# Kernel tuning notes

Measured on AMD Instinct MI355X. Metric: run time of the kernel, lower is better.

The kernel has to match this reference:

```python
import jax, jax.numpy as jnp
import numpy as np

C = 8.0


def _linear_scan(alpha, xbeta):
    # h_t = alpha_t * h_{t-1} + xbeta_t, scan over time axis=1
    def combine(e1, e2):
        a1, b1 = e1
        a2, b2 = e2
        return a2 * a1, a2 * b1 + b2
    _, h = jax.lax.associative_scan(combine, (alpha, xbeta), axis=1)
    return h


def setup_inputs() -> dict:
    dim = 2048
    B, T = 4, 4096
    key = jax.random.key(0)
    k_x, k_wi, k_wg = jax.random.split(key, 3)
    std = dim ** -0.5
    x = jax.random.normal(k_x, (B, T, dim), dtype=jnp.float32)
    W_in = jax.random.normal(k_wi, (dim, dim), dtype=jnp.float32) * std
    b_in = jnp.zeros((dim,), dtype=jnp.float32)
    W_gate = jax.random.normal(k_wg, (dim, dim), dtype=jnp.float32) * std
    b_gate = jnp.zeros((dim,), dtype=jnp.float32)
    forget_lambda = jnp.linspace(-4.323, -9.0, dim, dtype=jnp.float32)
    return {"x": x, "W_in": W_in, "b_in": b_in, "W_gate": W_gate,
            "b_gate": b_gate, "forget_lambda": forget_lambda}


def reference(x, W_in, b_in, W_gate, b_gate, forget_lambda):
    # x: [B, T, D]
    input_gate = jnp.einsum('btd,ed->bte', x, W_in) + b_in
    recurrence_gate = jnp.einsum('btd,ed->bte', x, W_gate) + b_gate
    # alpha_t = exp(-C * softplus(lambda) * sigmoid(r_t))  per channel
    alpha = jnp.exp(-C * jax.nn.softplus(forget_lambda) * jax.nn.sigmoid(recurrence_gate))
    beta = jnp.sqrt(1.0 - alpha ** 2 + 1e-6)
    xbeta = beta * jax.nn.sigmoid(input_gate) * x
    return _linear_scan(alpha, xbeta)
```

## Files before the change

kernel.cpp:

```cpp
#include <hip/hip_runtime.h>

typedef unsigned short u16;
typedef unsigned int u32;

using bf16x8 = __attribute__((ext_vector_type(8))) __bf16;
using f32x4  = __attribute__((ext_vector_type(4))) float;
using u16x8  = __attribute__((ext_vector_type(8))) u16;

#define BB 4
#define TT 4096
#define DD 2048
#define MM 16384
#define KK 2048
#define NCHUNK 16
#define CLEN 256

__device__ __forceinline__ u16 f2bf(float f) {
    u32 u = __float_as_uint(f);
    u32 r = (u + 0x7FFFu + ((u >> 16) & 1u)) >> 16;
    return (u16)r;
}

__device__ __forceinline__ void gload_lds16(const void* g, void* l) {
    __builtin_amdgcn_global_load_lds(
        (const __attribute__((address_space(1))) void*)g,
        (__attribute__((address_space(3))) void*)l, 16, 0, 0);
}

__global__ __launch_bounds__(256) void cvt_kernel(const float* __restrict__ in,
                                                  u16* __restrict__ out, int n8) {
    int i = blockIdx.x * 256 + threadIdx.x;
    if (i >= n8) return;
    const f32x4* p = (const f32x4*)in + (size_t)i * 2;
    f32x4 a = p[0], b = p[1];
    u16x8 o;
    o[0] = f2bf(a[0]); o[1] = f2bf(a[1]); o[2] = f2bf(a[2]); o[3] = f2bf(a[3]);
    o[4] = f2bf(b[0]); o[5] = f2bf(b[1]); o[6] = f2bf(b[2]); o[7] = f2bf(b[3]);
    *((u16x8*)out + i) = o;
}

#define BM 128
#define BN 128
#define BKg 32

__global__ __launch_bounds__(512) void gemm_dual(
    const u16* __restrict__ xb, const u16* __restrict__ wib, const u16* __restrict__ wgb,
    const float* __restrict__ xf,
    const float* __restrict__ b_in, const float* __restrict__ b_gate,
    const float* __restrict__ lam, u32* __restrict__ pair)
{
    __shared__ u16 As[BM * BKg];
    __shared__ u16 Bi[BN * BKg];
    __shared__ u16 Bg[BN * BKg];

    int tid = threadIdx.x;
    int bid = blockIdx.x;
    int cpx = gridDim.x >> 3;
    int swz = (bid & 7) * cpx + (bid >> 3);
    int et = swz & 15;
    int mt = swz >> 4;

    size_t m0 = (size_t)mt * BM;
    size_t e0 = (size_t)et * BN;

    int lane = tid & 63;
    int wid = tid >> 6;
    int wr  = wid >> 2;
    int wc  = wid & 3;

    int srow = tid >> 2;
    int skp  = (tid & 3) << 3;
    const u16* ga = xb  + (m0 + srow) * KK + skp;
    const u16* gi = wib + (e0 + srow) * KK + skp;
    const u16* gg = wgb + (e0 + srow) * KK + skp;
    u16* la = &As[tid * 8];
    u16* li = &Bi[tid * 8];
    u16* lg = &Bg[tid * 8];

    f32x4 accI[4][2], accG[4][2];
#pragma unroll
    for (int i = 0; i < 4; i++)
#pragma unroll
        for (int j = 0; j < 2; j++) {
            accI[i][j] = (f32x4){0.f, 0.f, 0.f, 0.f};
            accG[i][j] = (f32x4){0.f, 0.f, 0.f, 0.f};
        }

    int rowIn16 = lane & 15;
    int ksel = (lane >> 4) << 3;

    for (int k0 = 0; k0 < KK; k0 += BKg) {
        gload_lds16(ga, la);
        gload_lds16(gi, li);
        gload_lds16(gg, lg);
        ga += BKg; gi += BKg; gg += BKg;
        __syncthreads();

        bf16x8 aF[4], iF[2], gF[2];
#pragma unroll
        for (int mi = 0; mi < 4; mi++)
            aF[mi] = *(const bf16x8*)&As[(wr * 64 + mi * 16 + rowIn16) * BKg + ksel];
#pragma unroll
        for (int ni = 0; ni < 2; ni++) {
            iF[ni] = *(const bf16x8*)&Bi[(wc * 32 + ni * 16 + rowIn16) * BKg + ksel];
            gF[ni] = *(const bf16x8*)&Bg[(wc * 32 + ni * 16 + rowIn16) * BKg + ksel];
        }
#pragma unroll
        for (int mi = 0; mi < 4; mi++)
#pragma unroll
            for (int ni = 0; ni < 2; ni++) {
                accI[mi][ni] = __builtin_amdgcn_mfma_f32_16x16x32_bf16(aF[mi], iF[ni], accI[mi][ni], 0, 0, 0);
                accG[mi][ni] = __builtin_amdgcn_mfma_f32_16x16x32_bf16(aF[mi], gF[ni], accG[mi][ni], 0, 0, 0);
            }
        __syncthreads();
    }

    float spl[2], biv[2], bgv[2];
    size_t ecol[2];
#pragma unroll
    for (int ni = 0; ni < 2; ni++) {
        size_t e = e0 + wc * 32 + ni * 16 + rowIn16;
        ecol[ni] = e;
        spl[ni] = 8.0f * log1pf(__expf(lam[e]));
        biv[ni] = b_in[e];
        bgv[ni] = b_gate[e];
    }
    int rbase = (lane >> 4) * 4;
#pragma unroll
    for (int mi = 0; mi < 4; mi++) {
#pragma unroll
        for (int r = 0; r < 4; r++) {
            size_t m = m0 + wr * 64 + mi * 16 + rbase + r;
#pragma unroll
            for (int ni = 0; ni < 2; ni++) {
                size_t e = ecol[ni];
                float ig = accI[mi][ni][r] + biv[ni];
                float rg = accG[mi][ni][r] + bgv[ni];
                float sigr = 1.f / (1.f + __expf(-rg));
                float g = spl[ni] * sigr;
                float beta = sqrtf(1.f - __expf(-2.f * g) + 1e-6f);
                float xv = xf[m * DD + e];
                float xbeta = beta * (1.f / (1.f + __expf(-ig))) * xv;
                u32 pk = (u32)f2bf(g) | (((u32)f2bf(xbeta)) << 16);
                pair[m * DD + e] = pk;
            }
        }
    }
}

__global__ __launch_bounds__(256) void scanA(const u32* __restrict__ pair,
                                             float* __restrict__ aggG,
                                             float* __restrict__ aggB) {
    int gid = blockIdx.x * 256 + threadIdx.x;
    int e = gid & (DD - 1);
    int rest = gid >> 11;
    int b = rest & 3;
    int c = rest >> 2;
    const u32* p = pair + ((size_t)(b * TT + c * CLEN)) * DD + e;
    float gsum = 0.f, h = 0.f;
#pragma unroll 4
    for (int t = 0; t < CLEN; ++t) {
        u32 v = *p; p += DD;
        float gf = __uint_as_float(v << 16);
        float xbv = __uint_as_float(v & 0xFFFF0000u);
        gsum += gf;
        h = fmaf(__expf(-gf), h, xbv);
    }
    int idx = ((b * NCHUNK + c) << 11) | e;
    aggG[idx] = gsum;
    aggB[idx] = h;
}

__global__ __launch_bounds__(256) void scanB(const float* __restrict__ aggG,
                                             const float* __restrict__ aggB,
                                             float* __restrict__ carry) {
    int gid = blockIdx.x * 256 + threadIdx.x;
    int e = gid & (DD - 1);
    int b = gid >> 11;
    float h = 0.f;
#pragma unroll
    for (int c = 0; c < NCHUNK; ++c) {
        int idx = ((b * NCHUNK + c) << 11) | e;
        carry[idx] = h;
        h = fmaf(__expf(-aggG[idx]), h, aggB[idx]);
    }
}

__global__ __launch_bounds__(256) void scanC(const u32* __restrict__ pair,
                                             const float* __restrict__ carry,
                                             float* __restrict__ out) {
    int gid = blockIdx.x * 256 + threadIdx.x;
    int e = gid & (DD - 1);
    int rest = gid >> 11;
    int b = rest & 3;
    int c = rest >> 2;
    const u32* p = pair + ((size_t)(b * TT + c * CLEN)) * DD + e;
    float* o = out + ((size_t)(b * TT + c * CLEN)) * DD + e;
    float h = carry[((b * NCHUNK + c) << 11) | e];
#pragma unroll 4
    for (int t = 0; t < CLEN; ++t) {
        u32 v = *p; p += DD;
        float gf = __uint_as_float(v << 16);
        float xbv = __uint_as_float(v & 0xFFFF0000u);
        h = fmaf(__expf(-gf), h, xbv);
        *o = h; o += DD;
    }
}

extern "C" void kernel_launch(void* const* d_in, const int* in_sizes, int n_in,
                              void* d_out, int out_size, void* d_ws, size_t ws_size,
                              hipStream_t stream) {
    const float* x      = (const float*)d_in[0];
    const float* W_in   = (const float*)d_in[1];
    const float* b_in   = (const float*)d_in[2];
    const float* W_gate = (const float*)d_in[3];
    const float* b_gate = (const float*)d_in[4];
    const float* lam    = (const float*)d_in[5];
    float* out = (float*)d_out;

    char* ws = (char*)d_ws;
    u16* xb   = (u16*)(ws);
    u16* wib  = (u16*)(ws + 67108864);
    u16* wgb  = (u16*)(ws + 75497472);
    u32* pair = (u32*)(ws + 83886080);
    float* aggG  = (float*)(ws + 218103808);
    float* aggB  = (float*)(ws + 218628096);
    float* carry = (float*)(ws + 219152384);

    cvt_kernel<<<16384, 256, 0, stream>>>(x, xb, MM * KK / 8);
    cvt_kernel<<<2048, 256, 0, stream>>>(W_in, wib, DD * KK / 8);
    cvt_kernel<<<2048, 256, 0, stream>>>(W_gate, wgb, DD * KK / 8);
    gemm_dual<<<(MM / BM) * (DD / BN), 512, 0, stream>>>(xb, wib, wgb, x, b_in, b_gate, lam, pair);
    scanA<<<BB * DD * NCHUNK / 256, 256, 0, stream>>>(pair, aggG, aggB);
    scanB<<<BB * DD / 256, 256, 0, stream>>>(aggG, aggB, carry);
    scanC<<<BB * DD * NCHUNK / 256, 256, 0, stream>>>(pair, carry, out);
}
```

Before: 491.7 us.

## Rewrite dual GEMM with 4-stage LDS pipeline, larger M tile, swizzle

Replaces the single-buffered dual GEMM with a 256x128 tile that keeps a 4-deep ring of LDS buffers. Loads run three k-steps ahead, waits use explicit vmcnt/lgkmcnt counts, and each k-step's MFMA work is split into two halves that interleave with the async loads. The LDS layout is XOR-swizzled to avoid bank conflicts, and s_setprio is raised around the MFMA blocks. The aim is to hide global-load latency and raise the MFMA share of the loop. The cost is more LDS and registers per block (launch bounds ask for 2 blocks per CU) and fragile hand-placed wait counts.

```diff
diff --git a/kernel.cpp b/kernel.cpp
--- a/kernel.cpp
+++ b/kernel.cpp
@@ -26,6 +26,12 @@
         (const __attribute__((address_space(1))) void*)g,
         (__attribute__((address_space(3))) void*)l, 16, 0, 0);
 }
+
+#define BAR() do { __builtin_amdgcn_sched_barrier(0); __builtin_amdgcn_s_barrier(); __builtin_amdgcn_sched_barrier(0); } while(0)
+#define WAIT_LGKM0() do { asm volatile("s_waitcnt lgkmcnt(0)" ::: "memory"); __builtin_amdgcn_sched_barrier(0); } while(0)
+#define WAIT_VM8() do { asm volatile("s_waitcnt vmcnt(8)" ::: "memory"); __builtin_amdgcn_sched_barrier(0); } while(0)
+#define WAIT_VM4() do { asm volatile("s_waitcnt vmcnt(4)" ::: "memory"); __builtin_amdgcn_sched_barrier(0); } while(0)
+#define WAIT_VM0() do { asm volatile("s_waitcnt vmcnt(0)" ::: "memory"); __builtin_amdgcn_sched_barrier(0); } while(0)
 
 __global__ __launch_bounds__(256) void cvt_kernel(const float* __restrict__ in,
                                                   u16* __restrict__ out, int n8) {
@@ -39,98 +45,130 @@
     *((u16x8*)out + i) = o;
 }
 
-#define BM 128
-#define BN 128
+#define BMg 256
+#define BNg 128
 #define BKg 32
-
-__global__ __launch_bounds__(512) void gemm_dual(
+#define NT (KK / BKg)
+
+__global__ __launch_bounds__(512, 2) void gemm_dual8(
     const u16* __restrict__ xb, const u16* __restrict__ wib, const u16* __restrict__ wgb,
     const float* __restrict__ xf,
     const float* __restrict__ b_in, const float* __restrict__ b_gate,
     const float* __restrict__ lam, u32* __restrict__ pair)
 {
-    __shared__ u16 As[BM * BKg];
-    __shared__ u16 Bi[BN * BKg];
-    __shared__ u16 Bg[BN * BKg];
-
-    int tid = threadIdx.x;
-    int bid = blockIdx.x;
-    int cpx = gridDim.x >> 3;
-    int swz = (bid & 7) * cpx + (bid >> 3);
-    int et = swz & 15;
-    int mt = swz >> 4;
-
-    size_t m0 = (size_t)mt * BM;
-    size_t e0 = (size_t)et * BN;
-
-    int lane = tid & 63;
-    int wid = tid >> 6;
-    int wr  = wid >> 2;
-    int wc  = wid & 3;
-
-    int srow = tid >> 2;
-    int skp  = (tid & 3) << 3;
-    const u16* ga = xb  + (m0 + srow) * KK + skp;
-    const u16* gi = wib + (e0 + srow) * KK + skp;
-    const u16* gg = wgb + (e0 + srow) * KK + skp;
-    u16* la = &As[tid * 8];
-    u16* li = &Bi[tid * 8];
-    u16* lg = &Bg[tid * 8];
-
-    f32x4 accI[4][2], accG[4][2];
-#pragma unroll
-    for (int i = 0; i < 4; i++)
+    __shared__ u16 As[4][BMg * BKg];
+    __shared__ u16 Bs[4][2][BNg * BKg];
+
+    const int tid = threadIdx.x;
+    const int bid = blockIdx.x;
+    const int cpx = gridDim.x >> 3;
+    const int swz = (bid & 7) * cpx + (bid >> 3);
+    const int et = swz & 15;
+    const int mt = swz >> 4;
+    const size_t m0 = (size_t)mt * BMg;
+    const size_t e0 = (size_t)et * BNg;
+
+    const int lane = tid & 63;
+    const int wid = tid >> 6;
+    const int wr = wid >> 2;
+    const int wc = wid & 3;
+    const int r15 = lane & 15;
+    const int s4 = lane >> 4;
+
+    const int srow = tid >> 2;
+    const int sseg = (tid & 3) ^ ((tid >> 3) & 3);
+    const int skp  = sseg << 3;
+
+    const int koff = ((s4 ^ ((r15 >> 1) & 3)) << 3);
+
+#define STAGE_A(t) do { int _b = (t) & 3; size_t _k = (size_t)(t) * BKg + skp; \
+        gload_lds16(xb + (m0 + srow) * KK + _k,        &As[_b][tid * 8]); \
+        gload_lds16(xb + (m0 + 128 + srow) * KK + _k,  &As[_b][4096 + tid * 8]); } while (0)
+#define STAGE_B(t) do { int _b = (t) & 3; size_t _k = (size_t)(t) * BKg + skp; \
+        gload_lds16(wib + (e0 + srow) * KK + _k, &Bs[_b][0][tid * 8]); \
+        gload_lds16(wgb + (e0 + srow) * KK + _k, &Bs[_b][1][tid * 8]); } while (0)
+
+    f32x4 accI[8][2], accG[8][2];
+#pragma unroll
+    for (int i = 0; i < 8; i++)
 #pragma unroll
         for (int j = 0; j < 2; j++) {
             accI[i][j] = (f32x4){0.f, 0.f, 0.f, 0.f};
             accG[i][j] = (f32x4){0.f, 0.f, 0.f, 0.f};
         }
 
-    int rowIn16 = lane & 15;
-    int ksel = (lane >> 4) << 3;
-
-    for (int k0 = 0; k0 < KK; k0 += BKg) {
-        gload_lds16(ga, la);
-        gload_lds16(gi, li);
-        gload_lds16(gg, lg);
-        ga += BKg; gi += BKg; gg += BKg;
-        __syncthreads();
-
-        bf16x8 aF[4], iF[2], gF[2];
-#pragma unroll
-        for (int mi = 0; mi < 4; mi++)
-            aF[mi] = *(const bf16x8*)&As[(wr * 64 + mi * 16 + rowIn16) * BKg + ksel];
+    STAGE_A(0); STAGE_B(0);
+    STAGE_A(1); STAGE_B(1);
+    STAGE_A(2); STAGE_B(2);
+    WAIT_VM8();
+    BAR();
+
+    for (int t = 0; t < NT; ++t) {
+        const int cb = t & 3;
+        const u16* Ab = &As[cb][0];
+        const u16* BiB = &Bs[cb][0][0];
+        const u16* BgB = &Bs[cb][1][0];
+        bf16x8 bI[2], bG[2], aF[4];
+
+#pragma unroll
+        for (int q = 0; q < 4; q++)
+            aF[q] = *(const bf16x8*)&Ab[(wr * 128 + q * 16 + r15) * BKg + koff];
 #pragma unroll
         for (int ni = 0; ni < 2; ni++) {
-            iF[ni] = *(const bf16x8*)&Bi[(wc * 32 + ni * 16 + rowIn16) * BKg + ksel];
-            gF[ni] = *(const bf16x8*)&Bg[(wc * 32 + ni * 16 + rowIn16) * BKg + ksel];
+            bI[ni] = *(const bf16x8*)&BiB[(wc * 32 + ni * 16 + r15) * BKg + koff];
+            bG[ni] = *(const bf16x8*)&BgB[(wc * 32 + ni * 16 + r15) * BKg + koff];
         }
-#pragma unroll
-        for (int mi = 0; mi < 4; mi++)
+        if (t < NT - 3) STAGE_A(t + 3);
+        BAR();
+        WAIT_LGKM0();
+        __builtin_amdgcn_s_setprio(1);
+#pragma unroll
+        for (int q = 0; q < 4; q++)
 #pragma unroll
             for (int ni = 0; ni < 2; ni++) {
-                accI[mi][ni] = __builtin_amdgcn_mfma_f32_16x16x32_bf16(aF[mi], iF[ni], accI[mi][ni], 0, 0, 0);
-                accG[mi][ni] = __builtin_amdgcn_mfma_f32_16x16x32_bf16(aF[mi], gF[ni], accG[mi][ni], 0, 0, 0);
+                accI[q][ni] = __builtin_amdgcn_mfma_f32_16x16x32_bf16(aF[q], bI[ni], accI[q][ni], 0, 0, 0);
+                accG[q][ni] = __builtin_amdgcn_mfma_f32_16x16x32_bf16(aF[q], bG[ni], accG[q][ni], 0, 0, 0);
             }
-        __syncthreads();
+        __builtin_amdgcn_s_setprio(0);
+        BAR();
+
+#pragma unroll
+        for (int q = 0; q < 4; q++)
+            aF[q] = *(const bf16x8*)&Ab[(wr * 128 + (q + 4) * 16 + r15) * BKg + koff];
+        if (t < NT - 3) STAGE_B(t + 3);
+        BAR();
+        WAIT_LGKM0();
+        __builtin_amdgcn_s_setprio(1);
+#pragma unroll
+        for (int q = 0; q < 4; q++)
+#pragma unroll
+            for (int ni = 0; ni < 2; ni++) {
+                accI[q + 4][ni] = __builtin_amdgcn_mfma_f32_16x16x32_bf16(aF[q], bI[ni], accI[q + 4][ni], 0, 0, 0);
+                accG[q + 4][ni] = __builtin_amdgcn_mfma_f32_16x16x32_bf16(aF[q], bG[ni], accG[q + 4][ni], 0, 0, 0);
+            }
+        __builtin_amdgcn_s_setprio(0);
+        if (t < NT - 3)      WAIT_VM8();
+        else if (t == NT - 3) WAIT_VM4();
+        else                  WAIT_VM0();
+        BAR();
     }
 
     float spl[2], biv[2], bgv[2];
     size_t ecol[2];
 #pragma unroll
     for (int ni = 0; ni < 2; ni++) {
-        size_t e = e0 + wc * 32 + ni * 16 + rowIn16;
+        size_t e = e0 + wc * 32 + ni * 16 + r15;
         ecol[ni] = e;
         spl[ni] = 8.0f * log1pf(__expf(lam[e]));
         biv[ni] = b_in[e];
         bgv[ni] = b_gate[e];
     }
-    int rbase = (lane >> 4) * 4;
-#pragma unroll
-    for (int mi = 0; mi < 4; mi++) {
+    const int rbase = s4 * 4;
+#pragma unroll
+    for (int mi = 0; mi < 8; mi++) {
 #pragma unroll
         for (int r = 0; r < 4; r++) {
-            size_t m = m0 + wr * 64 + mi * 16 + rbase + r;
+            size_t m = m0 + wr * 128 + mi * 16 + rbase + r;
 #pragma unroll
             for (int ni = 0; ni < 2; ni++) {
                 size_t e = ecol[ni];
@@ -146,6 +184,8 @@
             }
         }
     }
+#undef STAGE_A
+#undef STAGE_B
 }
 
 __global__ __launch_bounds__(256) void scanA(const u32* __restrict__ pair,
@@ -230,7 +270,7 @@
     cvt_kernel<<<16384, 256, 0, stream>>>(x, xb, MM * KK / 8);
     cvt_kernel<<<2048, 256, 0, stream>>>(W_in, wib, DD * KK / 8);
     cvt_kernel<<<2048, 256, 0, stream>>>(W_gate, wgb, DD * KK / 8);
-    gemm_dual<<<(MM / BM) * (DD / BN), 512, 0, stream>>>(xb, wib, wgb, x, b_in, b_gate, lam, pair);
+    gemm_dual8<<<(MM / BMg) * (DD / BNg), 512, 0, stream>>>(xb, wib, wgb, x, b_in, b_gate, lam, pair);
     scanA<<<BB * DD * NCHUNK / 256, 256, 0, stream>>>(pair, aggG, aggB);
     scanB<<<BB * DD / 256, 256, 0, stream>>>(aggG, aggB, carry);
     scanC<<<BB * DD * NCHUNK / 256, 256, 0, stream>>>(pair, carry, out);
```

New measurement: 503.5 us. 2.4% more time.

## Interleave gate weights into one concatenated GEMM with 256x256 double-buffered tiles

Applied to the files above, without the earlier changes.

The two weight matrices are converted into a single interleaved bf16 matrix, so the dual GEMM becomes one GEMM of width 4096. It uses 256x256 tiles with a K step of 64, double-buffered LDS stages with an XOR swizzle, and a scheduled MFMA/LDS-read interleave. The epilogue pairs input-gate and recurrence-gate columns through a lane shuffle and reads x from the bf16 copy instead of the fp32 input. This aims at more data reuse per LDS load and fewer barriers. In exchange it needs large LDS (128KB) and many registers, which can limit occupancy, and x is now rounded to bf16 in the xbeta term.

```diff
diff --git a/kernel.cpp b/kernel.cpp
--- a/kernel.cpp
+++ b/kernel.cpp
@@ -12,6 +12,7 @@
 #define DD 2048
 #define MM 16384
 #define KK 2048
+#define NN 4096
 #define NCHUNK 16
 #define CLEN 256
 
@@ -39,113 +40,152 @@
     *((u16x8*)out + i) = o;
 }
 
-#define BM 128
-#define BN 128
-#define BKg 32
-
-__global__ __launch_bounds__(512) void gemm_dual(
-    const u16* __restrict__ xb, const u16* __restrict__ wib, const u16* __restrict__ wgb,
-    const float* __restrict__ xf,
+__global__ __launch_bounds__(256) void cvtw_kernel(const float* __restrict__ in,
+                                                   u16* __restrict__ out, int gate) {
+    int i = blockIdx.x * 256 + threadIdx.x;
+    int row = i >> 8;
+    int col8 = i & 255;
+    const f32x4* p = (const f32x4*)in + (size_t)i * 2;
+    f32x4 a = p[0], b = p[1];
+    u16x8 o;
+    o[0] = f2bf(a[0]); o[1] = f2bf(a[1]); o[2] = f2bf(a[2]); o[3] = f2bf(a[3]);
+    o[4] = f2bf(b[0]); o[5] = f2bf(b[1]); o[6] = f2bf(b[2]); o[7] = f2bf(b[3]);
+    size_t oidx = (((size_t)row * 2 + gate) << 11) + (size_t)col8 * 8;
+    *(u16x8*)(out + oidx) = o;
+}
+
+#define BKc 64
+#define NT (KK / BKc)
+
+#define MF(a_, b_, c_) __builtin_amdgcn_mfma_f32_16x16x32_bf16(a_, b_, c_, 0, 0, 0)
+#define MFMA8(Aa_, Ab_, B0_, B1_, B2_, B3_, ma_, mb_) do { \
+    acc[ma_][0] = MF(Aa_, B0_, acc[ma_][0]); \
+    acc[ma_][1] = MF(Aa_, B1_, acc[ma_][1]); \
+    acc[ma_][2] = MF(Aa_, B2_, acc[ma_][2]); \
+    acc[ma_][3] = MF(Aa_, B3_, acc[ma_][3]); \
+    acc[mb_][0] = MF(Ab_, B0_, acc[mb_][0]); \
+    acc[mb_][1] = MF(Ab_, B1_, acc[mb_][1]); \
+    acc[mb_][2] = MF(Ab_, B2_, acc[mb_][2]); \
+    acc[mb_][3] = MF(Ab_, B3_, acc[mb_][3]); \
+} while (0)
+
+__global__ __launch_bounds__(512, 2) void gemm_cat(
+    const u16* __restrict__ xb, const u16* __restrict__ wc,
     const float* __restrict__ b_in, const float* __restrict__ b_gate,
     const float* __restrict__ lam, u32* __restrict__ pair)
 {
-    __shared__ u16 As[BM * BKg];
-    __shared__ u16 Bi[BN * BKg];
-    __shared__ u16 Bg[BN * BKg];
-
-    int tid = threadIdx.x;
-    int bid = blockIdx.x;
-    int cpx = gridDim.x >> 3;
-    int swz = (bid & 7) * cpx + (bid >> 3);
-    int et = swz & 15;
-    int mt = swz >> 4;
-
-    size_t m0 = (size_t)mt * BM;
-    size_t e0 = (size_t)et * BN;
-
-    int lane = tid & 63;
-    int wid = tid >> 6;
-    int wr  = wid >> 2;
-    int wc  = wid & 3;
-
-    int srow = tid >> 2;
-    int skp  = (tid & 3) << 3;
-    const u16* ga = xb  + (m0 + srow) * KK + skp;
-    const u16* gi = wib + (e0 + srow) * KK + skp;
-    const u16* gg = wgb + (e0 + srow) * KK + skp;
-    u16* la = &As[tid * 8];
-    u16* li = &Bi[tid * 8];
-    u16* lg = &Bg[tid * 8];
-
-    f32x4 accI[4][2], accG[4][2];
-#pragma unroll
-    for (int i = 0; i < 4; i++)
-#pragma unroll
-        for (int j = 0; j < 2; j++) {
-            accI[i][j] = (f32x4){0.f, 0.f, 0.f, 0.f};
-            accG[i][j] = (f32x4){0.f, 0.f, 0.f, 0.f};
-        }
-
-    int rowIn16 = lane & 15;
-    int ksel = (lane >> 4) << 3;
-
-    for (int k0 = 0; k0 < KK; k0 += BKg) {
-        gload_lds16(ga, la);
-        gload_lds16(gi, li);
-        gload_lds16(gg, lg);
-        ga += BKg; gi += BKg; gg += BKg;
-        __syncthreads();
-
-        bf16x8 aF[4], iF[2], gF[2];
-#pragma unroll
-        for (int mi = 0; mi < 4; mi++)
-            aF[mi] = *(const bf16x8*)&As[(wr * 64 + mi * 16 + rowIn16) * BKg + ksel];
-#pragma unroll
-        for (int ni = 0; ni < 2; ni++) {
-            iF[ni] = *(const bf16x8*)&Bi[(wc * 32 + ni * 16 + rowIn16) * BKg + ksel];
-            gF[ni] = *(const bf16x8*)&Bg[(wc * 32 + ni * 16 + rowIn16) * BKg + ksel];
-        }
-#pragma unroll
-        for (int mi = 0; mi < 4; mi++)
-#pragma unroll
-            for (int ni = 0; ni < 2; ni++) {
-                accI[mi][ni] = __builtin_amdgcn_mfma_f32_16x16x32_bf16(aF[mi], iF[ni], accI[mi][ni], 0, 0, 0);
-                accG[mi][ni] = __builtin_amdgcn_mfma_f32_16x16x32_bf16(aF[mi], gF[ni], accG[mi][ni], 0, 0, 0);
-            }
-        __syncthreads();
-    }
-
-    float spl[2], biv[2], bgv[2];
-    size_t ecol[2];
-#pragma unroll
-    for (int ni = 0; ni < 2; ni++) {
-        size_t e = e0 + wc * 32 + ni * 16 + rowIn16;
-        ecol[ni] = e;
-        spl[ni] = 8.0f * log1pf(__expf(lam[e]));
-        biv[ni] = b_in[e];
-        bgv[ni] = b_gate[e];
-    }
-    int rbase = (lane >> 4) * 4;
-#pragma unroll
-    for (int mi = 0; mi < 4; mi++) {
-#pragma unroll
-        for (int r = 0; r < 4; r++) {
-            size_t m = m0 + wr * 64 + mi * 16 + rbase + r;
-#pragma unroll
-            for (int ni = 0; ni < 2; ni++) {
-                size_t e = ecol[ni];
-                float ig = accI[mi][ni][r] + biv[ni];
-                float rg = accG[mi][ni][r] + bgv[ni];
+    __shared__ u16 As[2][256 * BKc];
+    __shared__ u16 Bs[2][256 * BKc];
+
+    const int tid = threadIdx.x;
+    const int bid = blockIdx.x;
+    const int cpx = gridDim.x >> 3;
+    const int swz = (bid & 7) * cpx + (bid >> 3);
+    const int nt = swz & 15;
+    const int mt = swz >> 4;
+    const size_t m0 = (size_t)mt * 256;
+    const size_t n0 = (size_t)nt * 256;
+
+    const int lane = tid & 63;
+    const int wid = tid >> 6;
+    const int wr = wid >> 2;
+    const int wcv = (wid & 3) * 64;
+    const int r15 = lane & 15;
+    const int s4 = lane >> 4;
+
+    const u16* gA[4];
+    const u16* gB[4];
+#pragma unroll
+    for (int i = 0; i < 4; i++) {
+        int c = i * 512 + tid;
+        int r = c >> 3, seg = c & 7;
+        int segp = seg ^ (r & 7);
+        gA[i] = xb + (m0 + r) * (size_t)KK + segp * 8;
+        gB[i] = wc + (n0 + r) * (size_t)KK + segp * 8;
+    }
+
+#define STAGE(t) do { int _b = (t) & 1; size_t _k = (size_t)(t) * BKc; \
+        _Pragma("unroll") for (int i = 0; i < 4; i++) \
+            gload_lds16(gA[i] + _k, &As[_b][(i * 512 + tid) * 8]); \
+        _Pragma("unroll") for (int i = 0; i < 4; i++) \
+            gload_lds16(gB[i] + _k, &Bs[_b][(i * 512 + tid) * 8]); } while (0)
+
+    int kx[2];
+#pragma unroll
+    for (int ks = 0; ks < 2; ks++) kx[ks] = (((ks * 4 + s4) ^ (r15 & 7)) << 3);
+    int arow[8], brow[4];
+#pragma unroll
+    for (int mi = 0; mi < 8; mi++) arow[mi] = (wr * 128 + mi * 16 + r15) << 6;
+#pragma unroll
+    for (int ni = 0; ni < 4; ni++) brow[ni] = (wcv + ni * 16 + r15) << 6;
+
+#define RA(mi_, ks_) (*(const bf16x8*)&Ab[arow[mi_] + kx[ks_]])
+#define RB(ni_, ks_) (*(const bf16x8*)&Bb[brow[ni_] + kx[ks_]])
+
+    f32x4 acc[8][4];
+#pragma unroll
+    for (int i = 0; i < 8; i++)
+#pragma unroll
+        for (int j = 0; j < 4; j++) acc[i][j] = (f32x4){0.f, 0.f, 0.f, 0.f};
+
+    STAGE(0);
+
+#define ITER(t_, bi_) do { \
+        asm volatile("s_waitcnt vmcnt(0)" ::: "memory"); \
+        __builtin_amdgcn_s_barrier(); \
+        if ((t_) + 1 < NT) STAGE((t_) + 1); \
+        const u16* Ab = &As[bi_][0]; \
+        const u16* Bb = &Bs[bi_][0]; \
+        bf16x8 b0, b1, b2, b3, c0, c1, c2, c3, x0, x1, y0, y1; \
+        b0 = RB(0, 0); b1 = RB(1, 0); b2 = RB(2, 0); b3 = RB(3, 0); \
+        x0 = RA(0, 0); x1 = RA(1, 0); \
+        y0 = RA(2, 0); y1 = RA(3, 0);  MFMA8(x0, x1, b0, b1, b2, b3, 0, 1); \
+        x0 = RA(4, 0); x1 = RA(5, 0);  MFMA8(y0, y1, b0, b1, b2, b3, 2, 3); \
+        y0 = RA(6, 0); y1 = RA(7, 0);  MFMA8(x0, x1, b0, b1, b2, b3, 4, 5); \
+        c0 = RB(0, 1); c1 = RB(1, 1); c2 = RB(2, 1); c3 = RB(3, 1); \
+        x0 = RA(0, 1); x1 = RA(1, 1);  MFMA8(y0, y1, b0, b1, b2, b3, 6, 7); \
+        y0 = RA(2, 1); y1 = RA(3, 1);  MFMA8(x0, x1, c0, c1, c2, c3, 0, 1); \
+        x0 = RA(4, 1); x1 = RA(5, 1);  MFMA8(y0, y1, c0, c1, c2, c3, 2, 3); \
+        y0 = RA(6, 1); y1 = RA(7, 1);  MFMA8(x0, x1, c0, c1, c2, c3, 4, 5); \
+                                       MFMA8(y0, y1, c0, c1, c2, c3, 6, 7); \
+    } while (0)
+
+    for (int tt = 0; tt < NT; tt += 2) {
+        ITER(tt, 0);
+        ITER(tt + 1, 1);
+    }
+
+    const int gate = r15 & 1;
+#pragma unroll
+    for (int ni = 0; ni < 4; ni++) {
+        size_t n = n0 + wcv + ni * 16 + r15;
+        size_t ch = n >> 1;
+        float spl = 8.0f * log1pf(__expf(lam[ch]));
+        float biv = b_in[ch];
+        float bgv = b_gate[ch];
+#pragma unroll
+        for (int mi = 0; mi < 8; mi++) {
+#pragma unroll
+            for (int r = 0; r < 4; r++) {
+                float own = acc[mi][ni][r];
+                float oth = __shfl_xor(own, 1, 64);
+                float ig = (gate ? oth : own) + biv;
+                float rg = (gate ? own : oth) + bgv;
                 float sigr = 1.f / (1.f + __expf(-rg));
-                float g = spl[ni] * sigr;
+                float g = spl * sigr;
                 float beta = sqrtf(1.f - __expf(-2.f * g) + 1e-6f);
-                float xv = xf[m * DD + e];
+                size_t m = m0 + wr * 128 + mi * 16 + s4 * 4 + r;
+                float xv = __uint_as_float((u32)xb[m * KK + ch] << 16);
                 float xbeta = beta * (1.f / (1.f + __expf(-ig))) * xv;
                 u32 pk = (u32)f2bf(g) | (((u32)f2bf(xbeta)) << 16);
-                pair[m * DD + e] = pk;
+                if (!gate) pair[m * DD + ch] = pk;
             }
         }
     }
+#undef STAGE
+#undef RA
+#undef RB
+#undef ITER
 }
 
 __global__ __launch_bounds__(256) void scanA(const u32* __restrict__ pair,
@@ -220,17 +260,16 @@
 
     char* ws = (char*)d_ws;
     u16* xb   = (u16*)(ws);
-    u16* wib  = (u16*)(ws + 67108864);
-    u16* wgb  = (u16*)(ws + 75497472);
+    u16* wc   = (u16*)(ws + 67108864);
     u32* pair = (u32*)(ws + 83886080);
     float* aggG  = (float*)(ws + 218103808);
     float* aggB  = (float*)(ws + 218628096);
     float* carry = (float*)(ws + 219152384);
 
     cvt_kernel<<<16384, 256, 0, stream>>>(x, xb, MM * KK / 8);
-    cvt_kernel<<<2048, 256, 0, stream>>>(W_in, wib, DD * KK / 8);
-    cvt_kernel<<<2048, 256, 0, stream>>>(W_gate, wgb, DD * KK / 8);
-    gemm_dual<<<(MM / BM) * (DD / BN), 512, 0, stream>>>(xb, wib, wgb, x, b_in, b_gate, lam, pair);
+    cvtw_kernel<<<2048, 256, 0, stream>>>(W_in, wc, 0);
+    cvtw_kernel<<<2048, 256, 0, stream>>>(W_gate, wc, 1);
+    gemm_cat<<<(MM / 256) * (NN / 256), 512, 0, stream>>>(xb, wc, b_in, b_gate, lam, pair);
     scanA<<<BB * DD * NCHUNK / 256, 256, 0, stream>>>(pair, aggG, aggB);
     scanB<<<BB * DD / 256, 256, 0, stream>>>(aggG, aggB, carry);
     scanC<<<BB * DD * NCHUNK / 256, 256, 0, stream>>>(pair, carry, out);
```

Result: slower. 607.2 us (+23.5%).
